# Kernel optimization log

Measured on AMD Instinct MI355X. Metric: run time of the kernel, lower is better.

## Reference

```python
import jax, jax.numpy as jnp
import numpy as np
from jax import lax

DN = ('NHWC', 'HWIO', 'NHWC')
EPS = 1e-3  # keras BatchNormalization default epsilon


def conv2d(x, w):
    return lax.conv_general_dilated(x, w, (1, 1), 'SAME', dimension_numbers=DN)


def convlstm2d(x, W, U, b):
    # x: (B,T,H,Wd,Cin); W: (kh,kw,Cin,4F); U: (kh,kw,F,4F); b: (4F,)
    # Keras ConvLSTM2D, gate order i,f,c,o; recurrent_activation=sigmoid, activation=relu
    B, T, H, Wd, _ = x.shape
    F = U.shape[2]
    xz = conv2d(x.reshape(B * T, H, Wd, -1), W).reshape(B, T, H, Wd, 4 * F) + b

    def step(carry, xt):
        h, c = carry
        z = xt + conv2d(h, U)
        i, f, g, o = jnp.split(z, 4, axis=-1)
        i = jax.nn.sigmoid(i)
        f = jax.nn.sigmoid(f)
        c = f * c + i * jax.nn.relu(g)
        h = jax.nn.sigmoid(o) * jax.nn.relu(c)
        return (h, c), h

    h0 = jnp.zeros((B, H, Wd, F), x.dtype)
    _, hs = lax.scan(step, (h0, h0), jnp.moveaxis(xz, 0, 1))  # (T,B,H,W,F)
    return jnp.moveaxis(hs, 0, 1)


def batchnorm(x, gamma, beta, mean, var):
    return (x - mean) * (gamma * lax.rsqrt(var + EPS)) + beta


def maxpool_122(x):
    # MaxPooling3D pool=(1,2,2), strides=(1,2,2), padding='same', channels_last
    return lax.reduce_window(x, -jnp.inf, lax.max, (1, 1, 2, 2, 1), (1, 1, 2, 2, 1), 'SAME')


def setup_inputs() -> dict:
    key = jax.random.key(0)
    ks = iter(jax.random.split(key, 32))
    s = 0.05
    d = {
        'x': jax.random.normal(next(ks), (8, 10, 64, 64, 3), jnp.float32),
        'W1': jax.random.normal(next(ks), (5, 5, 3, 128), jnp.float32) * s,
        'U1': jax.random.normal(next(ks), (5, 5, 32, 128), jnp.float32) * s,
        'b1': jnp.zeros((128,), jnp.float32),
        'g1': jax.random.uniform(next(ks), (32,), jnp.float32, 0.5, 1.5),
        'be1': jax.random.normal(next(ks), (32,), jnp.float32) * 0.1,
        'm1': jax.random.normal(next(ks), (32,), jnp.float32) * 0.1,
        'v1': jax.random.uniform(next(ks), (32,), jnp.float32, 0.5, 1.5),
        'W2': jax.random.normal(next(ks), (5, 5, 32, 128), jnp.float32) * s,
        'U2': jax.random.normal(next(ks), (5, 5, 32, 128), jnp.float32) * s,
        'b2': jnp.zeros((128,), jnp.float32),
        'g2': jax.random.uniform(next(ks), (32,), jnp.float32, 0.5, 1.5),
        'be2': jax.random.normal(next(ks), (32,), jnp.float32) * 0.1,
        'm2': jax.random.normal(next(ks), (32,), jnp.float32) * 0.1,
        'v2': jax.random.uniform(next(ks), (32,), jnp.float32, 0.5, 1.5),
        'W3': jax.random.normal(next(ks), (3, 3, 32, 128), jnp.float32) * s,
        'U3': jax.random.normal(next(ks), (3, 3, 32, 128), jnp.float32) * s,
        'b3': jnp.zeros((128,), jnp.float32),
        'g3': jax.random.uniform(next(ks), (32,), jnp.float32, 0.5, 1.5),
        'be3': jax.random.normal(next(ks), (32,), jnp.float32) * 0.1,
        'm3': jax.random.normal(next(ks), (32,), jnp.float32) * 0.1,
        'v3': jax.random.uniform(next(ks), (32,), jnp.float32, 0.5, 1.5),
        'Wd1': jax.random.normal(next(ks), (20480, 64), jnp.float32) * 0.01,
        'bd1': jnp.zeros((64,), jnp.float32),
        'Wd2': jax.random.normal(next(ks), (64, 10), jnp.float32) * 0.1,
        'bd2': jnp.zeros((10,), jnp.float32),
    }
    return d


def reference(x, W1, U1, b1, g1, be1, m1, v1, W2, U2, b2, g2, be2, m2, v2,
              W3, U3, b3, g3, be3, m3, v3, Wd1, bd1, Wd2, bd2):
    x = convlstm2d(x, W1, U1, b1)
    x = maxpool_122(batchnorm(x, g1, be1, m1, v1))
    x = convlstm2d(x, W2, U2, b2)
    x = maxpool_122(batchnorm(x, g2, be2, m2, v2))
    x = convlstm2d(x, W3, U3, b3)
    x = maxpool_122(batchnorm(x, g3, be3, m3, v3))
    x = x.reshape(x.shape[0], -1)  # (B, T*H*W*F) = (8, 20480)
    x = jax.nn.softmax(x @ Wd1 + bd1, axis=-1)
    return jax.nn.softmax(x @ Wd2 + bd2, axis=-1)
```

## Files before the change

### kernel.cpp

```cpp
#include <hip/hip_runtime.h>

using short8 = __attribute__((ext_vector_type(8))) short;
using f32x4  = __attribute__((ext_vector_type(4))) float;

__device__ __forceinline__ unsigned short f2bf(float x){
    unsigned u = __float_as_uint(x);
    unsigned r = (u + 0x7FFFu + ((u>>16)&1u)) >> 16;
    return (unsigned short)r;
}
__device__ __forceinline__ float bf2f(unsigned short h){
    return __uint_as_float(((unsigned)h)<<16);
}
__device__ __forceinline__ float sigf(float x){ return 1.0f/(1.0f+__expf(-x)); }
__device__ __forceinline__ int swz(int b){ return b ^ (((b>>7)&7)<<4); }

struct SP {
    const float *x;
    const float *g1,*be1,*m1,*v1;
    const float *g2,*be2,*m2,*v2;
    const float *g3,*be3,*m3,*v3;
    unsigned short *hs1,*hs2,*hs3;
    unsigned short *pl1,*pl2,*pl3;
    float *cst1,*cst2,*cst3;
    const short8 *U1b,*W1b,*U2b,*W2b,*U3b,*W3b;
    const float *bp;
};

__global__ __launch_bounds__(256)
void xform_all(const float* __restrict__ U1, const float* __restrict__ W1,
               const float* __restrict__ U2, const float* __restrict__ W2,
               const float* __restrict__ U3, const float* __restrict__ W3,
               const float* __restrict__ b1, const float* __restrict__ b2, const float* __restrict__ b3,
               short8* __restrict__ U1b, short8* __restrict__ W1b,
               short8* __restrict__ U2b, short8* __restrict__ W2b,
               short8* __restrict__ U3b, short8* __restrict__ W3b,
               float* __restrict__ bp)
{
    int i = blockIdx.x*256 + threadIdx.x;
    if (i >= 49536) return;
    if (i >= 49152) {
        int j = i - 49152, layer = j >> 7, np = j & 127;
        int oc = ((np>>4)&3)*32 + (np>>6)*16 + (np&15);
        const float* bs = layer==0 ? b1 : (layer==1 ? b2 : b3);
        bp[j] = bs[oc];
        return;
    }
    const float* src; short8* dst; int base, kmax;
    if      (i < 12800){ src=U1; dst=U1b; base=0;     kmax=800; }
    else if (i < 14336){ src=W1; dst=W1b; base=12800; kmax=75;  }
    else if (i < 27136){ src=U2; dst=U2b; base=14336; kmax=800; }
    else if (i < 39936){ src=W2; dst=W2b; base=27136; kmax=800; }
    else if (i < 44544){ src=U3; dst=U3b; base=39936; kmax=288; }
    else               { src=W3; dst=W3b; base=44544; kmax=288; }
    int j = i - base;
    int lane = j & 63, nt = (j >> 6) & 7, tap = j >> 9;
    int np = nt*16 + (lane & 15);
    int oc = ((np>>4)&3)*32 + (np>>6)*16 + (np&15);
    int g = lane >> 4;
    short8 pk;
    #pragma unroll
    for (int e = 0; e < 8; ++e) {
        int k = tap*32 + g*8 + e;
        unsigned short v = (k < kmax) ? f2bf(src[(long)k*128 + oc]) : (unsigned short)0;
        pk[e] = (short)v;
    }
    dst[j] = pk;
}

template<int K, int PW, int MT2>
__device__ __forceinline__ void conv_taps(f32x4 (&acc)[MT2][4],
    const unsigned short* patch, const short8* Wf, int mh, int nh, int l15, int g4, int lane)
{
    constexpr int NTAP = K*K;
    const short8* ub = Wf + nh*4*64 + lane;
    short8 bA0 = ub[0], bA1 = ub[64], bA2 = ub[128], bA3 = ub[192];
    short8 bB0 = bA0, bB1 = bA1, bB2 = bA2, bB3 = bA3;
    { const short8* u = ub + 512; bB0=u[0]; bB1=u[64]; bB2=u[128]; bB3=u[192]; }
    #pragma unroll 1
    for (int tp = 0; tp < NTAP; tp += 2) {
        {
            int dy = tp / K, dx = tp % K;
            #pragma unroll
            for (int mt = 0; mt < MT2; ++mt) {
                short8 af = *(const short8*)((const char*)patch +
                    swz(((mh*MT2 + mt + dy)*PW + l15 + dx)*64 + g4*16));
                acc[mt][0] = __builtin_amdgcn_mfma_f32_16x16x32_bf16(af, bA0, acc[mt][0], 0,0,0);
                acc[mt][1] = __builtin_amdgcn_mfma_f32_16x16x32_bf16(af, bA1, acc[mt][1], 0,0,0);
                acc[mt][2] = __builtin_amdgcn_mfma_f32_16x16x32_bf16(af, bA2, acc[mt][2], 0,0,0);
                acc[mt][3] = __builtin_amdgcn_mfma_f32_16x16x32_bf16(af, bA3, acc[mt][3], 0,0,0);
            }
            if (tp + 2 < NTAP) { const short8* u = ub + (long)(tp+2)*512; bA0=u[0];bA1=u[64];bA2=u[128];bA3=u[192]; }
        }
        if (tp + 1 < NTAP) {
            int dy = (tp+1) / K, dx = (tp+1) % K;
            #pragma unroll
            for (int mt = 0; mt < MT2; ++mt) {
                short8 af = *(const short8*)((const char*)patch +
                    swz(((mh*MT2 + mt + dy)*PW + l15 + dx)*64 + g4*16));
                acc[mt][0] = __builtin_amdgcn_mfma_f32_16x16x32_bf16(af, bB0, acc[mt][0], 0,0,0);
                acc[mt][1] = __builtin_amdgcn_mfma_f32_16x16x32_bf16(af, bB1, acc[mt][1], 0,0,0);
                acc[mt][2] = __builtin_amdgcn_mfma_f32_16x16x32_bf16(af, bB2, acc[mt][2], 0,0,0);
                acc[mt][3] = __builtin_amdgcn_mfma_f32_16x16x32_bf16(af, bB3, acc[mt][3], 0,0,0);
            }
            if (tp + 3 < NTAP) { const short8* u = ub + (long)(tp+3)*512; bB0=u[0];bB1=u[64];bB2=u[128];bB3=u[192]; }
        }
    }
}

template<int MT2>
__device__ __forceinline__ void lstm_epilogue(
    f32x4 (&acc)[MT2][4], unsigned short* hs, float* cst, unsigned short* plout,
    const float* gg, const float* bb, const float* mm, const float* vv,
    int H, int W, int n, int y0, int x0, int t, int mh, int nh, int l15, int g4, int first)
{
    const int f = nh*16 + l15;
    const int xt = x0 >> 4;
    const float sc = gg[f] * rsqrtf(vv[f] + 1e-3f);
    const float sh = bb[f] - mm[f]*sc;
    unsigned short* outh = hs + ((long)n*10 + t)*(long)H*W*32;
    float hv[MT2][4];
    #pragma unroll
    for (int mt = 0; mt < MT2; ++mt) {
        int row = y0 + mh*MT2 + mt;
        long tb = ((long)(n*H + row)*(W>>4) + xt)*512 + f*16 + g4*4;
        f32x4 cold = first ? (f32x4){0.f,0.f,0.f,0.f} : *(const f32x4*)&cst[tb];
        f32x4 cn;
        #pragma unroll
        for (int j = 0; j < 4; ++j) {
            float zi = acc[mt][0][j];
            float zf = acc[mt][1][j];
            float zg = acc[mt][2][j];
            float zo = acc[mt][3][j];
            float c2 = sigf(zf)*cold[j] + sigf(zi)*fmaxf(zg, 0.0f);
            cn[j] = c2;
            float h = sigf(zo)*fmaxf(c2, 0.0f);
            hv[mt][j] = h;
            outh[((long)row*W + (x0 + g4*4 + j))*32 + f] = f2bf(h);
        }
        *(f32x4*)&cst[tb] = cn;
    }
    #pragma unroll
    for (int mp = 0; mp < MT2/2; ++mp) {
        int orow = (y0>>1) + mh*(MT2/2) + mp;
        #pragma unroll
        for (int jp = 0; jp < 2; ++jp) {
            int ocol = (x0>>1) + g4*2 + jp;
            float mx = fmaxf(fmaxf(hv[2*mp][2*jp],   hv[2*mp][2*jp+1]),
                             fmaxf(hv[2*mp+1][2*jp], hv[2*mp+1][2*jp+1]));
            plout[(((long)(n*10 + t)*(H>>1) + orow)*(W>>1) + ocol)*32 + f] = f2bf(mx*sc + sh);
        }
    }
}

__device__ void l1_step(char* smem, const SP& p, int n, int y0, int x0, int t)
{
    constexpr int PAD = 2, PH = 8, PW = 20, MT2 = 2, MPX = 64;
    const int H = 64, W = 64;
    unsigned short* patch_s = (unsigned short*)smem;
    unsigned short* xpk_s   = (unsigned short*)(smem + 10240);
    const int tid = threadIdx.x;
    const int lane = tid & 63, wid = tid >> 6;
    const int mh = wid >> 1, nh = wid & 1;
    const int l15 = lane & 15, g4 = lane >> 4;
    const int first = (t == 0);

    short8 z8 = {0,0,0,0,0,0,0,0};
    #pragma unroll
    for (int c = tid; c < MPX*96/8; c += 256)
        ((short8*)xpk_s)[c] = z8;

    if (!first) {
        const unsigned short* s = p.hs1 + ((long)n*10 + (t-1))*(long)H*W*32;
        #pragma unroll 2
        for (int c = tid; c < PH*PW*4; c += 256) {
            int pix = c >> 2, gq = c & 3;
            int pr = pix / PW, pc = pix % PW;
            int gy = y0 - PAD + pr, gx = x0 - PAD + pc;
            short8 v = z8;
            if ((unsigned)gy < 64u && (unsigned)gx < 64u)
                v = *(const short8*)(s + ((long)gy*W + gx)*32 + gq*8);
            *(short8*)((char*)patch_s + swz(pix*64 + gq*16)) = v;
        }
    }
    __syncthreads();
    {
        const float* xs = p.x + ((long)n*10 + t)*4096*3;
        const int px = tid & 63;
        const int prow = px >> 4, pcol = px & 15;
        #pragma unroll 2
        for (int tap = tid >> 6; tap < 25; tap += 4) {
            int dy = (tap*52) >> 8, dx = tap - dy*5;
            int gy = y0 + prow - PAD + dy;
            int gx = x0 + pcol - PAD + dx;
            float v0=0.f, v1=0.f, v2=0.f;
            if ((unsigned)gy < 64u && (unsigned)gx < 64u) {
                const float* b = xs + ((long)gy*64 + gx)*3;
                v0 = b[0]; v1 = b[1]; v2 = b[2];
            }
            int o = px*192 + tap*6;
            *(unsigned short*)((char*)xpk_s + swz(o))   = f2bf(v0);
            *(unsigned short*)((char*)xpk_s + swz(o+2)) = f2bf(v1);
            *(unsigned short*)((char*)xpk_s + swz(o+4)) = f2bf(v2);
        }
    }
    __syncthreads();

    f32x4 acc[MT2][4];
    #pragma unroll
    for (int ntl = 0; ntl < 4; ++ntl) {
        float bv = p.bp[(nh*4+ntl)*16 + l15];
        #pragma unroll
        for (int mt = 0; mt < MT2; ++mt)
            acc[mt][ntl] = (f32x4){bv,bv,bv,bv};
    }
    #pragma unroll 1
    for (int c = 0; c < 3; ++c) {
        const short8* wp = p.W1b + ((long)c*8 + nh*4)*64 + lane;
        short8 bf0 = wp[0], bf1 = wp[64], bf2 = wp[128], bf3 = wp[192];
        #pragma unroll
        for (int mt = 0; mt < MT2; ++mt) {
            short8 af = *(const short8*)((const char*)xpk_s +
                swz(((mh*MT2+mt)*16 + l15)*192 + c*64 + g4*16));
            acc[mt][0] = __builtin_amdgcn_mfma_f32_16x16x32_bf16(af, bf0, acc[mt][0], 0,0,0);
            acc[mt][1] = __builtin_amdgcn_mfma_f32_16x16x32_bf16(af, bf1, acc[mt][1], 0,0,0);
            acc[mt][2] = __builtin_amdgcn_mfma_f32_16x16x32_bf16(af, bf2, acc[mt][2], 0,0,0);
            acc[mt][3] = __builtin_amdgcn_mfma_f32_16x16x32_bf16(af, bf3, acc[mt][3], 0,0,0);
        }
    }
    if (!first)
        conv_taps<5,PW,MT2>(acc, patch_s, p.U1b, mh, nh, l15, g4, lane);

    lstm_epilogue<MT2>(acc, p.hs1, p.cst1, p.pl1, p.g1, p.be1, p.m1, p.v1,
                       H, W, n, y0, x0, t, mh, nh, l15, g4, first);
}

template<int K, int HH>
__device__ void l23_step(char* smem, const SP& p,
    unsigned short* hs, const unsigned short* plin, unsigned short* plout, float* cst,
    const short8* Ufr, const short8* Wfr, const float* bp,
    const float* gg, const float* bb, const float* mm, const float* vv,
    int n, int y0, int x0, int t)
{
    constexpr int TH = 4, PAD = K/2, PH = TH+K-1, PW = 16+K-1, MT2 = 2;
    const int H = HH, W = HH;
    unsigned short* patchH = (unsigned short*)smem;
    unsigned short* patchX = (unsigned short*)(smem + PH*PW*64);

    const int tid = threadIdx.x;
    const int lane = tid & 63, wid = tid >> 6;
    const int mh = wid >> 1, nh = wid & 1;
    const int l15 = lane & 15, g4 = lane >> 4;
    const int first = (t == 0);

    const unsigned short* hsrc = hs + ((long)n*10 + (t-1))*(long)H*W*32;
    const unsigned short* xsrc = plin + ((long)n*10 + t)*(long)H*W*32;
    short8 z8 = {0,0,0,0,0,0,0,0};
    #pragma unroll 2
    for (int c = tid; c < PH*PW*4; c += 256) {
        int pix = c >> 2, gq = c & 3;
        int pr = pix / PW, pc = pix % PW;
        int gy = y0 - PAD + pr, gx = x0 - PAD + pc;
        short8 vx = z8, vh = z8;
        if ((unsigned)gy < (unsigned)H && (unsigned)gx < (unsigned)W) {
            vx = *(const short8*)(xsrc + ((long)gy*W + gx)*32 + gq*8);
            if (!first) vh = *(const short8*)(hsrc + ((long)gy*W + gx)*32 + gq*8);
        }
        *(short8*)((char*)patchX + swz(pix*64 + gq*16)) = vx;
        *(short8*)((char*)patchH + swz(pix*64 + gq*16)) = vh;
    }
    __syncthreads();

    f32x4 acc[MT2][4];
    #pragma unroll
    for (int ntl = 0; ntl < 4; ++ntl) {
        float bv = bp[(nh*4+ntl)*16 + l15];
        #pragma unroll
        for (int mt = 0; mt < MT2; ++mt)
            acc[mt][ntl] = (f32x4){bv,bv,bv,bv};
    }
    conv_taps<K,PW,MT2>(acc, patchX, Wfr, mh, nh, l15, g4, lane);
    if (!first) conv_taps<K,PW,MT2>(acc, patchH, Ufr, mh, nh, l15, g4, lane);

    lstm_epilogue<MT2>(acc, hs, cst, plout, gg, bb, mm, vv,
                       H, W, n, y0, x0, t, mh, nh, l15, g4, first);
}

__global__ __launch_bounds__(256, 2)
void stage_k(SP p, int s)
{
    __shared__ __align__(16) char smem[22528];
    const int bid = blockIdx.x;
    if (bid < 128) {
        int t = s - 1;
        if (t >= 0 && t < 10) {
            int n = bid >> 4, rem = bid & 15;
            l23_step<5,32>(smem, p, p.hs2, p.pl1, p.pl2, p.cst2,
                           p.U2b, p.W2b, p.bp + 128,
                           p.g2, p.be2, p.m2, p.v2,
                           n, (rem >> 1)*4, (rem & 1)*16, t);
        }
    } else if (bid < 160) {
        int t = s - 2;
        if (t >= 0 && t < 10) {
            int idx = bid - 128;
            int n = idx >> 2, rem = idx & 3;
            l23_step<3,16>(smem, p, p.hs3, p.pl2, p.pl3, p.cst3,
                           p.U3b, p.W3b, p.bp + 256,
                           p.g3, p.be3, p.m3, p.v3,
                           n, rem*4, 0, t);
        }
    } else {
        int t = s;
        if (t < 10) {
            int idx = bid - 160;
            int n = idx >> 6, rem = idx & 63;
            l1_step(smem, p, n, (rem >> 2)*4, (rem & 3)*16, t);
        }
    }
}

__global__ __launch_bounds__(256)
void dense_all(const unsigned short* __restrict__ flat, const float* __restrict__ Wd1,
               const float* __restrict__ bd1, const float* __restrict__ Wd2,
               const float* __restrict__ bd2, float* __restrict__ partial,
               unsigned* __restrict__ ctr, float* __restrict__ outp)
{
    __shared__ __align__(16) float xs[2048];
    __shared__ unsigned rank_s;
    const int kc = blockIdx.x, k0 = kc*256;
    const int t = threadIdx.x;
    {
        int r = t >> 5, kb = (t & 31)*8;
        short8 v = *(const short8*)(flat + (long)r*20480 + k0 + kb);
        #pragma unroll
        for (int e = 0; e < 8; ++e) xs[(kb+e)*8 + r] = bf2f((unsigned short)v[e]);
    }
    __syncthreads();
    const int c = t & 63, seg = t >> 6;
    f32x4 accA = {0,0,0,0}, accB = {0,0,0,0};
    #pragma unroll 4
    for (int kk = seg*64; kk < seg*64 + 64; ++kk) {
        float w = Wd1[(long)(k0+kk)*64 + c];
        f32x4 xa = *(const f32x4*)&xs[kk*8];
        f32x4 xb = *(const f32x4*)&xs[kk*8 + 4];
        #pragma unroll
        for (int j = 0; j < 4; ++j) { accA[j] = fmaf(xa[j], w, accA[j]); accB[j] = fmaf(xb[j], w, accB[j]); }
    }
    __syncthreads();
    #pragma unroll
    for (int j = 0; j < 4; ++j) {
        xs[(seg*8 + j)*64 + c]     = accA[j];
        xs[(seg*8 + 4 + j)*64 + c] = accB[j];
    }
    __syncthreads();
    #pragma unroll
    for (int o = t; o < 512; o += 256) {
        int r = o >> 6, cc = o & 63;
        partial[(long)kc*512 + o] = (xs[(0*8+r)*64+cc] + xs[(1*8+r)*64+cc])
                                  + (xs[(2*8+r)*64+cc] + xs[(3*8+r)*64+cc]);
    }
    __syncthreads();
    if (t == 0) {
        __builtin_amdgcn_fence(__ATOMIC_RELEASE, "agent");
        rank_s = __hip_atomic_fetch_add(ctr, 1u, __ATOMIC_ACQ_REL, __HIP_MEMORY_SCOPE_AGENT);
    }
    __syncthreads();
    if (rank_s != 79) return;
    __builtin_amdgcn_fence(__ATOMIC_ACQUIRE, "agent");

    float* d1  = xs;
    float* l2s = xs + 512;
    #pragma unroll
    for (int rr = 0; rr < 2; ++rr) {
        int idx = rr*256 + t;
        int cc = idx & 63;
        float s = bd1[cc];
        #pragma unroll 4
        for (int q = 0; q < 80; ++q) s += partial[q*512 + idx];
        float mx = s;
        for (int o = 32; o > 0; o >>= 1) mx = fmaxf(mx, __shfl_xor(mx, o, 64));
        float e = __expf(s - mx);
        float sm = e;
        for (int o = 32; o > 0; o >>= 1) sm += __shfl_xor(sm, o, 64);
        d1[idx] = e / sm;
    }
    __syncthreads();
    if (t < 80) {
        int r = t / 10, o = t % 10;
        float l = bd2[o];
        #pragma unroll 8
        for (int cc = 0; cc < 64; ++cc) l = fmaf(d1[r*64 + cc], Wd2[cc*10 + o], l);
        l2s[t] = l;
    }
    __syncthreads();
    if (t < 8) {
        float mx2 = l2s[t*10];
        #pragma unroll
        for (int j = 1; j < 10; ++j) mx2 = fmaxf(mx2, l2s[t*10 + j]);
        float ev[10], s2 = 0.f;
        #pragma unroll
        for (int j = 0; j < 10; ++j) { ev[j] = __expf(l2s[t*10 + j] - mx2); s2 += ev[j]; }
        #pragma unroll
        for (int j = 0; j < 10; ++j) outp[t*10 + j] = ev[j] / s2;
    }
}

extern "C" void kernel_launch(void* const* d_in, const int* in_sizes, int n_in,
                              void* d_out, int out_size, void* d_ws, size_t ws_size,
                              hipStream_t stream)
{
    const float* Wd1 = (const float*)d_in[22];
    const float* bd1 = (const float*)d_in[23];
    const float* Wd2 = (const float*)d_in[24];
    const float* bd2 = (const float*)d_in[25];

    char* ws = (char*)d_ws;
    SP p;
    p.x   = (const float*)d_in[0];
    p.g1  = (const float*)d_in[4];  p.be1 = (const float*)d_in[5];  p.m1 = (const float*)d_in[6];  p.v1 = (const float*)d_in[7];
    p.g2  = (const float*)d_in[11]; p.be2 = (const float*)d_in[12]; p.m2 = (const float*)d_in[13]; p.v2 = (const float*)d_in[14];
    p.g3  = (const float*)d_in[18]; p.be3 = (const float*)d_in[19]; p.m3 = (const float*)d_in[20]; p.v3 = (const float*)d_in[21];

    p.hs1 = (unsigned short*)(ws);
    p.hs2 = (unsigned short*)(ws + 20971520);
    p.hs3 = (unsigned short*)(ws + 26214400);
    p.cst1 = (float*)(ws + 27525120);
    p.cst2 = (float*)(ws + 31719424);
    p.cst3 = (float*)(ws + 32768000);
    p.pl1 = (unsigned short*)(ws + 33030144);
    p.pl2 = (unsigned short*)(ws + 38273024);
    p.pl3 = (unsigned short*)(ws + 39583744);
    short8* U1b = (short8*)(ws + 39911424);
    short8* W1b = (short8*)(ws + 40116224);
    short8* U2b = (short8*)(ws + 40140800);
    short8* W2b = (short8*)(ws + 40345600);
    short8* U3b = (short8*)(ws + 40550400);
    short8* W3b = (short8*)(ws + 40624128);
    float*  bp  = (float*)(ws + 40697856);
    float*  partial = (float*)(ws + 40699392);
    unsigned* ctr = (unsigned*)(ws + 40863232);
    p.U1b = U1b; p.W1b = W1b; p.U2b = U2b; p.W2b = W2b; p.U3b = U3b; p.W3b = W3b;
    p.bp = bp;

    hipMemsetAsync(ctr, 0, 64, stream);

    xform_all<<<194, 256, 0, stream>>>(
        (const float*)d_in[2], (const float*)d_in[1],
        (const float*)d_in[9], (const float*)d_in[8],
        (const float*)d_in[16], (const float*)d_in[15],
        (const float*)d_in[3], (const float*)d_in[10], (const float*)d_in[17],
        U1b, W1b, U2b, W2b, U3b, W3b, bp);

    for (int s = 0; s < 12; ++s)
        stage_k<<<672, 256, 0, stream>>>(p, s);

    dense_all<<<80, 256, 0, stream>>>(p.pl3, Wd1, bd1, Wd2, bd2, partial,
                                      ctr, (float*)d_out);
}
```

Baseline: 252.3 us.

## Enlarge layer-1 tiles, stage raw input in LDS, drop memset launch

Layer-1 blocks now cover 8x16 output pixels instead of 4x16, which halves their count and the total grid from 672 to 416 blocks. The input patch is loaded once from global memory into a raw bf16 LDS buffer and expanded into the im2col layout from LDS, replacing 25 strided global loads per pixel. The counter memset is folded into the first stage kernel as an atomic store, removing one launch. Shared memory per block grows to about 41 KB and the 2-blocks-per-SM launch bound is dropped, so occupancy may fall and layer-1 blocks now carry more work each.

Measured after the change: 224.6 us, median of 2. -11.0%, faster.

```diff
diff --git a/kernel.cpp b/kernel.cpp
--- a/kernel.cpp
+++ b/kernel.cpp
@@ -24,6 +24,7 @@
     float *cst1,*cst2,*cst3;
     const short8 *U1b,*W1b,*U2b,*W2b,*U3b,*W3b;
     const float *bp;
+    unsigned *ctr;
 };
 
 __global__ __launch_bounds__(256)
@@ -154,10 +155,11 @@
 
 __device__ void l1_step(char* smem, const SP& p, int n, int y0, int x0, int t)
 {
-    constexpr int PAD = 2, PH = 8, PW = 20, MT2 = 2, MPX = 64;
+    constexpr int PAD = 2, PH = 12, PW = 20, MT2 = 4, MPX = 128;
     const int H = 64, W = 64;
     unsigned short* patch_s = (unsigned short*)smem;
-    unsigned short* xpk_s   = (unsigned short*)(smem + 10240);
+    unsigned short* xpk_s   = (unsigned short*)(smem + 15360);
+    unsigned short* xraw    = (unsigned short*)(smem + 39936);
     const int tid = threadIdx.x;
     const int lane = tid & 63, wid = tid >> 6;
     const int mh = wid >> 1, nh = wid & 1;
@@ -169,9 +171,23 @@
     for (int c = tid; c < MPX*96/8; c += 256)
         ((short8*)xpk_s)[c] = z8;
 
+    if (tid < PH*PW) {
+        const float* xs = p.x + ((long)n*10 + t)*4096*3;
+        int gy = y0 - PAD + tid / PW;
+        int gx = x0 - PAD + tid % PW;
+        float v0=0.f, v1=0.f, v2=0.f;
+        if ((unsigned)gy < 64u && (unsigned)gx < 64u) {
+            const float* b = xs + ((long)gy*64 + gx)*3;
+            v0 = b[0]; v1 = b[1]; v2 = b[2];
+        }
+        xraw[tid*3]   = f2bf(v0);
+        xraw[tid*3+1] = f2bf(v1);
+        xraw[tid*3+2] = f2bf(v2);
+    }
+
     if (!first) {
         const unsigned short* s = p.hs1 + ((long)n*10 + (t-1))*(long)H*W*32;
-        #pragma unroll 2
+        #pragma unroll 1
         for (int c = tid; c < PH*PW*4; c += 256) {
             int pix = c >> 2, gq = c & 3;
             int pr = pix / PW, pc = pix % PW;
@@ -183,25 +199,16 @@
         }
     }
     __syncthreads();
-    {
-        const float* xs = p.x + ((long)n*10 + t)*4096*3;
-        const int px = tid & 63;
-        const int prow = px >> 4, pcol = px & 15;
-        #pragma unroll 2
-        for (int tap = tid >> 6; tap < 25; tap += 4) {
-            int dy = (tap*52) >> 8, dx = tap - dy*5;
-            int gy = y0 + prow - PAD + dy;
-            int gx = x0 + pcol - PAD + dx;
-            float v0=0.f, v1=0.f, v2=0.f;
-            if ((unsigned)gy < 64u && (unsigned)gx < 64u) {
-                const float* b = xs + ((long)gy*64 + gx)*3;
-                v0 = b[0]; v1 = b[1]; v2 = b[2];
-            }
-            int o = px*192 + tap*6;
-            *(unsigned short*)((char*)xpk_s + swz(o))   = f2bf(v0);
-            *(unsigned short*)((char*)xpk_s + swz(o+2)) = f2bf(v1);
-            *(unsigned short*)((char*)xpk_s + swz(o+4)) = f2bf(v2);
-        }
+
+    #pragma unroll 1
+    for (int c = tid; c < MPX*25; c += 256) {
+        int px = c & (MPX-1), tap = c >> 7;
+        int dy = (tap*52) >> 8, dx = tap - dy*5;
+        int pi = ((px>>4) + dy)*PW + (px&15) + dx;
+        int o = px*192 + tap*6;
+        *(unsigned short*)((char*)xpk_s + swz(o))   = xraw[pi*3];
+        *(unsigned short*)((char*)xpk_s + swz(o+2)) = xraw[pi*3+1];
+        *(unsigned short*)((char*)xpk_s + swz(o+4)) = xraw[pi*3+2];
     }
     __syncthreads();
 
@@ -255,7 +262,7 @@
     const unsigned short* hsrc = hs + ((long)n*10 + (t-1))*(long)H*W*32;
     const unsigned short* xsrc = plin + ((long)n*10 + t)*(long)H*W*32;
     short8 z8 = {0,0,0,0,0,0,0,0};
-    #pragma unroll 2
+    #pragma unroll 1
     for (int c = tid; c < PH*PW*4; c += 256) {
         int pix = c >> 2, gq = c & 3;
         int pr = pix / PW, pc = pix % PW;
@@ -285,36 +292,38 @@
                        H, W, n, y0, x0, t, mh, nh, l15, g4, first);
 }
 
-__global__ __launch_bounds__(256, 2)
+__global__ __launch_bounds__(256)
 void stage_k(SP p, int s)
 {
-    __shared__ __align__(16) char smem[22528];
+    __shared__ __align__(16) char smem[41472];
     const int bid = blockIdx.x;
-    if (bid < 128) {
+    if (bid < 256) {
+        int t = s;
+        if (t < 10) {
+            int n = bid >> 5, rem = bid & 31;
+            l1_step(smem, p, n, (rem >> 2)*8, (rem & 3)*16, t);
+        }
+    } else if (bid < 384) {
         int t = s - 1;
         if (t >= 0 && t < 10) {
-            int n = bid >> 4, rem = bid & 15;
+            int idx = bid - 256;
+            int n = idx >> 4, rem = idx & 15;
             l23_step<5,32>(smem, p, p.hs2, p.pl1, p.pl2, p.cst2,
                            p.U2b, p.W2b, p.bp + 128,
                            p.g2, p.be2, p.m2, p.v2,
                            n, (rem >> 1)*4, (rem & 1)*16, t);
-        }
-    } else if (bid < 160) {
+        } else if (s == 0 && bid == 256 && threadIdx.x == 0) {
+            __hip_atomic_store(p.ctr, 0u, __ATOMIC_RELEASE, __HIP_MEMORY_SCOPE_AGENT);
+        }
+    } else {
         int t = s - 2;
         if (t >= 0 && t < 10) {
-            int idx = bid - 128;
+            int idx = bid - 384;
             int n = idx >> 2, rem = idx & 3;
             l23_step<3,16>(smem, p, p.hs3, p.pl2, p.pl3, p.cst3,
                            p.U3b, p.W3b, p.bp + 256,
                            p.g3, p.be3, p.m3, p.v3,
                            n, rem*4, 0, t);
-        }
-    } else {
-        int t = s;
-        if (t < 10) {
-            int idx = bid - 160;
-            int n = idx >> 6, rem = idx & 63;
-            l1_step(smem, p, n, (rem >> 2)*4, (rem & 3)*16, t);
         }
     }
 }
@@ -438,11 +447,9 @@
     short8* W3b = (short8*)(ws + 40624128);
     float*  bp  = (float*)(ws + 40697856);
     float*  partial = (float*)(ws + 40699392);
-    unsigned* ctr = (unsigned*)(ws + 40863232);
+    p.ctr = (unsigned*)(ws + 40863232);
     p.U1b = U1b; p.W1b = W1b; p.U2b = U2b; p.W2b = W2b; p.U3b = U3b; p.W3b = W3b;
     p.bp = bp;
-
-    hipMemsetAsync(ctr, 0, 64, stream);
 
     xform_all<<<194, 256, 0, stream>>>(
         (const float*)d_in[2], (const float*)d_in[1],
@@ -452,8 +459,8 @@
         U1b, W1b, U2b, W2b, U3b, W3b, bp);
 
     for (int s = 0; s < 12; ++s)
-        stage_k<<<672, 256, 0, stream>>>(p, s);
+        stage_k<<<416, 256, 0, stream>>>(p, s);
 
     dense_all<<<80, 256, 0, stream>>>(p.pl3, Wd1, bd1, Wd2, bd2, partial,
-                                      ctr, (float*)d_out);
-}
+                                      p.ctr, (float*)d_out);
+}
```
